# Kernel optimization log

Hardware: AMD Instinct MI355X
Metric: run time of the kernel (lower is better)

## Reference

```python
import jax, jax.numpy as jnp
import numpy as np

B, C_IN, C_OUT, N, T = 16, 32, 64, 1024, 24
IN_DIM, S_DIM, D_DIM, K, KT = 1, 16, 16, 3, 3


def conv1x1(x, W, b):
    # x: [B,Ci,N,T], W: [Co,Ci], b: [Co] -> [B,Co,N,T]
    return jnp.einsum('oi,bint->bont', W, x) + b[None, :, None, None]


def conv_t(x, W, b):
    # temporal conv, kernel (1,KT), padding (0,1) -> length preserved
    out = jax.lax.conv_general_dilated(
        x, W, window_strides=(1, 1), padding=((0, 0), (1, 1)),
        dimension_numbers=('NCHW', 'OIHW', 'NCHW'))
    return out + b[None, :, None, None]


def coss_attn(Dv, y, Wq, bq, Wk, bk, Wv, bv):
    # cross-attention per node over the temporal axis: Q from y, K/V from Dv
    Q = conv1x1(y, Wq, bq)
    Kx = conv1x1(Dv, Wk, bk)
    V = conv1x1(Dv, Wv, bv)
    scale = 1.0 / jnp.sqrt(jnp.asarray(Q.shape[1], Q.dtype))
    A = jax.nn.softmax(jnp.einsum('bcnt,bcns->bnts', Q, Kx) * scale, axis=-1)
    return jnp.einsum('bnts,bcns->bcnt', A, V)


def cheby(x, supports, Wg, bg, k):
    # Chebyshev polynomial graph conv: T0=I, T1=L, T2=2L T1 - T0
    n = supports.shape[0]
    L0 = jnp.eye(n, dtype=x.dtype)
    L1 = supports
    Ls = [L0, L1]
    for _ in range(2, k):
        L2 = 2.0 * supports @ L1 - L0
        L0, L1 = L1, L2
        Ls.append(L2)
    Lap = jnp.stack(Ls, 0)  # [K,N,N]
    xk = jnp.einsum('kqn,bcnt->bckqt', Lap, x)  # aggregate neighbours
    bsz, c, kk, nn, tt = xk.shape
    xk = xk.reshape(bsz, c * kk, nn, tt)
    return conv1x1(xk, Wg, bg)


def setup_inputs() -> dict:
    key = jax.random.key(0)
    ks = jax.random.split(key, 32)
    s = 0.05
    inp = {
        'x': jax.random.normal(ks[0], (B, C_IN, N, T), jnp.float32),
        'supports': jax.random.normal(ks[1], (N, N), jnp.float32) / np.sqrt(N).astype(np.float32),
        'CD': jax.random.normal(ks[2], (N, D_DIM), jnp.float32),
        'CS': jax.random.normal(ks[3], (N, S_DIM), jnp.float32),
        'adj': jax.random.normal(ks[4], (N, N), jnp.float32) / np.sqrt(N).astype(np.float32),
        # DelayEstimators params
        'W_de': jax.random.normal(ks[5], (C_OUT, C_IN), jnp.float32) * s,
        'b_de': jnp.zeros((C_OUT,), jnp.float32),
        'Wd': jax.random.normal(ks[6], (D_DIM, T), jnp.float32) * s,
        # conv_pro
        'W_pro': jax.random.normal(ks[7], (IN_DIM, C_IN), jnp.float32) * s,
        'b_pro': jnp.zeros((IN_DIM,), jnp.float32),
        # MultiScaleGCN
        'W_mii': jax.random.normal(ks[8], (C_OUT, S_DIM), jnp.float32) * s,
        'b_mii': jnp.zeros((C_OUT,), jnp.float32),
        # conv_1 residual
        'W_1': jax.random.normal(ks[9], (C_OUT, C_IN), jnp.float32) * s,
        'b_1': jnp.zeros((C_OUT,), jnp.float32),
        # TSFN cross-attention (query from x with c_in channels)
        'Wq_t': jax.random.normal(ks[10], (C_OUT, C_IN), jnp.float32) * s,
        'bq_t': jnp.zeros((C_OUT,), jnp.float32),
        'Wk_t': jax.random.normal(ks[11], (C_OUT, C_OUT), jnp.float32) * s,
        'bk_t': jnp.zeros((C_OUT,), jnp.float32),
        'Wv_t': jax.random.normal(ks[12], (C_OUT, C_OUT), jnp.float32) * s,
        'bv_t': jnp.zeros((C_OUT,), jnp.float32),
        # conv1 temporal (1,Kt)
        'W_c1': jax.random.normal(ks[13], (C_OUT, C_OUT, 1, KT), jnp.float32) * s,
        'b_c1': jnp.zeros((C_OUT,), jnp.float32),
        # SSFN cross-attention
        'Wq_s': jax.random.normal(ks[14], (C_OUT, C_OUT), jnp.float32) * s,
        'bq_s': jnp.zeros((C_OUT,), jnp.float32),
        'Wk_s': jax.random.normal(ks[15], (C_OUT, C_OUT), jnp.float32) * s,
        'bk_s': jnp.zeros((C_OUT,), jnp.float32),
        'Wv_s': jax.random.normal(ks[16], (C_OUT, C_OUT), jnp.float32) * s,
        'bv_s': jnp.zeros((C_OUT,), jnp.float32),
        # cheby conv output projection (K*c_out -> 2*c_out)
        'W_g': jax.random.normal(ks[17], (2 * C_OUT, K * C_OUT), jnp.float32) * s,
        'b_g': jnp.zeros((2 * C_OUT,), jnp.float32),
    }
    return inp


def reference(x, supports, CD, CS, adj, W_de, b_de, Wd, W_pro, b_pro,
              W_mii, b_mii, W_1, b_1, Wq_t, bq_t, Wk_t, bk_t, Wv_t, bv_t,
              W_c1, b_c1, Wq_s, bq_s, Wk_s, bk_s, Wv_s, bv_s, W_g, b_g):
    # DelayEstimators: projected trend modulated by node-wise learned delay gate
    delay = jax.nn.sigmoid(jnp.tanh(CD @ Wd))            # [N,T]
    D = conv1x1(x, W_de, b_de) * delay[None, None, :, :]  # [B,c_out,N,T]
    # conv_pro + broadcast of spatial context CS
    u = conv1x1(x, W_pro, b_pro)[:, 0]                    # [B,N,T] (in_dim==1)
    CSb = jnp.einsum('bnt,ne->bent', u, CS)               # [B,S_dim,N,T]
    # MultiScaleGCN: 1x1 projection + adjacency aggregation (identity + adj)
    h = conv1x1(CSb, W_mii, b_mii)
    S = h + jnp.einsum('nm,bcmt->bcnt', adj, h)           # [B,c_out,N,T]
    x_input1 = conv1x1(x, W_1, b_1)
    XD = coss_attn(D, x, Wq_t, bq_t, Wk_t, bk_t, Wv_t, bv_t) + x_input1
    x1 = conv_t(XD, W_c1, b_c1)
    XS = coss_attn(S, x1, Wq_s, bq_s, Wk_s, bk_s, Wv_s, bv_s)
    x2 = cheby(XS, supports, W_g, b_g, K)                 # [B,2*c_out,N,T]
    filt, gate = x2[:, :C_OUT], x2[:, C_OUT:]
    return (filt + x_input1) * jax.nn.sigmoid(gate)
```

## Files before the change

kernel.cpp:

```cpp
#include <hip/hip_runtime.h>
#include <cstdint>
#include <cstddef>

#define B_    16
#define CIN_  32
#define COUT_ 64
#define N_    1024
#define T_    24
#define SD_   16
#define DD_   16

#define NT_      (N_*T_)
#define BNT_     (B_*N_*T_)
#define UE_COLS  (B_*T_*SD_)
#define XS_COLS  (B_*COUT_*T_)
#define HALF_COLS (XS_COLS/2)

typedef unsigned short ushort_t;
using bf16x8 = __attribute__((ext_vector_type(8))) short;
using f32x4  = __attribute__((ext_vector_type(4))) float;

#define OFF_DELAY 0ul
#define OFF_M     98304ul
#define OFF_R     360448ul
#define OFF_U     364544ul
#define OFF_W1T   1953792ul
#define OFF_WGBF  2048000ul
#define OFF_SBF   2195456ul
#define OFF_ADJBF 4292608ul
#define OFF_STBF  6389760ul
#define OFF_L2BF  8486912ul
#define OFF_X1    10584064ul
#define OFF_X2    23166976ul
#define OFF_XS    48332800ul
#define OFF_Y1H   98664448ul
#define OFF_Y2H   123830272ul
#define OFF_WBF   148996096ul

#define WB_DE   0
#define WB_QT   2048
#define WB_1    4096
#define WB_MIIA 6144
#define WB_KT   8192
#define WB_VT   12288
#define WB_QS   16384
#define WB_KS   20480
#define WB_VS   24576
#define WB_C1A  28672
#define WB_TOTAL 40960

__device__ __forceinline__ float bfb2f(ushort_t h) {
  union { unsigned u; float f; } v; v.u = ((unsigned)h) << 16; return v.f;
}
__device__ __forceinline__ ushort_t f2bfb(float f) {
  union { float f; unsigned u; } v; v.f = f;
  unsigned u = v.u;
  return (ushort_t)((u + 0x7fffu + ((u >> 16) & 1u)) >> 16);
}
__device__ __forceinline__ float sigm_(float z) { return 1.f / (1.f + expf(-z)); }

__device__ __forceinline__ void gl_lds16(const ushort_t* g, ushort_t* l) {
  __builtin_amdgcn_global_load_lds(
      (const __attribute__((address_space(1))) unsigned int*)g,
      (__attribute__((address_space(3))) unsigned int*)l, 16, 0, 0);
}

__device__ __forceinline__ void st4bf(ushort_t* p, float v0, float v1, float v2, float v3) {
  uint2 w;
  w.x = (unsigned)f2bfb(v0) | ((unsigned)f2bfb(v1) << 16);
  w.y = (unsigned)f2bfb(v2) | ((unsigned)f2bfb(v3) << 16);
  *(uint2*)p = w;
}

__global__ __launch_bounds__(256) void k_prep(
    const float* __restrict__ supports, const float* __restrict__ adj,
    const float* __restrict__ W_de, const float* __restrict__ Wq_t,
    const float* __restrict__ W_1, const float* __restrict__ W_mii,
    const float* __restrict__ Wk_t, const float* __restrict__ Wv_t,
    const float* __restrict__ Wq_s, const float* __restrict__ Wk_s,
    const float* __restrict__ Wv_s, const float* __restrict__ W_c1,
    const float* __restrict__ W_g,
    ushort_t* __restrict__ Sbf, ushort_t* __restrict__ adjbf,
    float* __restrict__ W1T, ushort_t* __restrict__ WGBF,
    ushort_t* __restrict__ WBF)
{
  int idx = blockIdx.x * 256 + threadIdx.x;
  if (idx < N_*N_) {
    Sbf[idx]   = f2bfb(supports[idx]);
    adjbf[idx] = f2bfb(adj[idx]);
  }
  int j = idx - N_*N_;
  if (j < 0) return;
  if (j < 2048) { int k = j>>6, c = j&63; W1T[j] = W_1[c*32 + k]; return; }
  j -= 2048;
  if (j < 24576) { WGBF[j] = f2bfb(W_g[j]); return; }
  j -= 24576;
  if (j < 2048) { WBF[WB_DE + j] = f2bfb(W_de[j]); return; }
  j -= 2048;
  if (j < 2048) { WBF[WB_QT + j] = f2bfb(Wq_t[j]); return; }
  j -= 2048;
  if (j < 2048) { WBF[WB_1 + j] = f2bfb(W_1[j]); return; }
  j -= 2048;
  if (j < 2048) { int c = j>>5, k = j&31;
                  WBF[WB_MIIA + j] = (k < 16) ? f2bfb(W_mii[c*16 + k]) : (ushort_t)0; return; }
  j -= 2048;
  if (j < 4096) { WBF[WB_KT + j] = f2bfb(Wk_t[j]); return; }
  j -= 4096;
  if (j < 4096) { WBF[WB_VT + j] = f2bfb(Wv_t[j]); return; }
  j -= 4096;
  if (j < 4096) { WBF[WB_QS + j] = f2bfb(Wq_s[j]); return; }
  j -= 4096;
  if (j < 4096) { WBF[WB_KS + j] = f2bfb(Wk_s[j]); return; }
  j -= 4096;
  if (j < 4096) { WBF[WB_VS + j] = f2bfb(Wv_s[j]); return; }
  j -= 4096;
  if (j < 12288) { int d = j >> 12, r = j & 4095, c = r >> 6, jj = r & 63;
                   WBF[WB_C1A + j] = f2bfb(W_c1[(c*64 + jj)*3 + d]); return; }
}
#define PREP_TOTAL (N_*N_ + 2048 + 24576 + WB_TOTAL)

__global__ __launch_bounds__(256) void k_pre(
    const float* __restrict__ CD, const float* __restrict__ Wd,
    const float* __restrict__ CS, const float* __restrict__ W_mii,
    const float* __restrict__ adj,
    float* __restrict__ delay, float* __restrict__ Mbuf, float* __restrict__ Rbuf)
{
  int idx = blockIdx.x * 256 + threadIdx.x;
  if (idx < NT_) {
    int n = idx / T_, t = idx % T_;
    float z = 0.f;
    #pragma unroll
    for (int d = 0; d < DD_; ++d) z += CD[n*DD_ + d] * Wd[d*T_ + t];
    delay[idx] = sigm_(tanhf(z));
  }
  int i2 = idx - NT_;
  if (i2 >= 0 && i2 < N_*COUT_) {
    int n = i2 / COUT_, c = i2 % COUT_;
    float z = 0.f;
    #pragma unroll
    for (int e = 0; e < SD_; ++e) z += CS[n*SD_ + e] * W_mii[c*SD_ + e];
    Mbuf[i2] = z;
  }
  int i3 = idx - NT_ - N_*COUT_;
  if (i3 >= 0 && i3 < 8*N_) {
    int n = i3 >> 3, jl = i3 & 7;
    const float* row = adj + (size_t)n * N_;
    float s = 0.f;
    for (int m = jl; m < N_; m += 8) s += row[m];
    s += __shfl_xor(s, 1);
    s += __shfl_xor(s, 2);
    s += __shfl_xor(s, 4);
    if (jl == 0) Rbuf[n] = s;
  }
}

__global__ __launch_bounds__(256) void k_u(
    const float* __restrict__ x, const float* __restrict__ W_pro,
    const float* __restrict__ b_pro, const float* __restrict__ CS,
    float* __restrict__ u, ushort_t* __restrict__ Ue)
{
  int idx = blockIdx.x * 256 + threadIdx.x;
  if (idx >= BNT_) return;
  int t = idx % T_;
  int n = (idx / T_) % N_;
  int b = idx / (T_ * N_);
  const float* xp = x + ((size_t)b * CIN_ * N_ + n) * T_ + t;
  float z = b_pro[0];
  #pragma unroll
  for (int i = 0; i < CIN_; ++i) z += W_pro[i] * xp[(size_t)i * NT_];
  u[idx] = z;
  ushort_t* up = Ue + (size_t)n * UE_COLS + (b * T_ + t) * SD_;
  #pragma unroll
  for (int e = 0; e < SD_; ++e) up[e] = f2bfb(z * CS[n*SD_ + e]);
}

__global__ __launch_bounds__(256) void k_tr(
    const ushort_t* __restrict__ src, ushort_t* __restrict__ dst,
    int R, int sstride)
{
  __shared__ ushort_t tb[32][33];
  const int tid = threadIdx.x;
  const int tx = tid & 31, ty = tid >> 5;
  const int c0 = blockIdx.x * 32, r0 = blockIdx.y * 32;
  #pragma unroll
  for (int p = 0; p < 4; ++p) {
    int r = r0 + ty + p*8;
    tb[ty + p*8][tx] = src[(size_t)r * sstride + c0 + tx];
  }
  __syncthreads();
  #pragma unroll
  for (int p = 0; p < 4; ++p) {
    int c = c0 + ty + p*8;
    dst[(size_t)c * R + r0 + tx] = tb[tx][ty + p*8];
  }
}

template<int MODE>
__global__ __launch_bounds__(256) void k_mmx(
    const ushort_t* __restrict__ Abf, const ushort_t* __restrict__ BT,
    ushort_t* __restrict__ Cc, int ncols)
{
  __shared__ ushort_t As[128*64];
  __shared__ ushort_t Bs[128*64];
  const int tid  = threadIdx.x;
  const int wave = tid >> 6, lane = tid & 63;
  const int row0 = blockIdx.y * 128;
  const int col0 = blockIdx.x * 128;
  const int wm = (wave >> 1) * 64, wn = (wave & 1) * 64;
  const int l15 = lane & 15, quad = lane >> 4, l7 = lane & 7;

  f32x4 acc[4][4];
  #pragma unroll
  for (int i = 0; i < 4; ++i)
    #pragma unroll
    for (int j = 0; j < 4; ++j) acc[i][j] = (f32x4){0.f,0.f,0.f,0.f};

  for (int kb = 0; kb < 1024; kb += 64) {
    #pragma unroll
    for (int p = 0; p < 4; ++p) {
      int chunk = p*256 + tid;
      int r = chunk >> 3, pc = chunk & 7;
      int kc = pc ^ (r & 7);
      gl_lds16(Abf + (size_t)(row0 + r)*1024 + (kb + kc*8), &As[chunk*8]);
    }
    #pragma unroll
    for (int p = 0; p < 4; ++p) {
      int chunk = p*256 + tid;
      int r = chunk >> 3, pc = chunk & 7;
      int kc = pc ^ (r & 7);
      gl_lds16(BT + (size_t)(col0 + r)*1024 + (kb + kc*8), &Bs[chunk*8]);
    }
    __syncthreads();
    #pragma unroll
    for (int kh = 0; kh < 2; ++kh) {
      const int kcb = kh * 4;
      bf16x8 af[4], bfr[4];
      #pragma unroll
      for (int mi = 0; mi < 4; ++mi)
        af[mi] = *(const bf16x8*)&As[(wm + mi*16 + l15)*64 + (((kcb + quad) ^ l7) << 3)];
      #pragma unroll
      for (int ni = 0; ni < 4; ++ni)
        bfr[ni] = *(const bf16x8*)&Bs[(wn + ni*16 + l15)*64 + (((kcb + quad) ^ l7) << 3)];
      #pragma unroll
      for (int mi = 0; mi < 4; ++mi)
        #pragma unroll
        for (int ni = 0; ni < 4; ++ni)
          acc[mi][ni] = __builtin_amdgcn_mfma_f32_16x16x32_bf16(
              af[mi], bfr[ni], acc[mi][ni], 0, 0, 0);
    }
    __syncthreads();
  }

  #pragma unroll
  for (int mi = 0; mi < 4; ++mi) {
    int grow_b = row0 + wm + mi*16 + quad*4;
    #pragma unroll
    for (int ni = 0; ni < 4; ++ni) {
      int gcol = col0 + wn + ni*16 + l15;
      #pragma unroll
      for (int j = 0; j < 4; ++j) {
        float v = acc[mi][ni][j];
        int grow = grow_b + j;
        if (MODE == 2) v = 2.f*v - ((grow == gcol) ? 1.f : 0.f);
        Cc[(size_t)grow * ncols + gcol] = f2bfb(v);
      }
    }
  }
}

__global__ __launch_bounds__(256) void k_mmy(
    const ushort_t* __restrict__ Sbf, const ushort_t* __restrict__ L2bf,
    const ushort_t* __restrict__ BT,
    ushort_t* __restrict__ Y1, ushort_t* __restrict__ Y2, int ncols)
{
  __shared__ ushort_t As[128*64];
  __shared__ ushort_t Bs[128*64];
  const int tid  = threadIdx.x;
  const int wave = tid >> 6, lane = tid & 63;
  const bool isY2 = blockIdx.y >= 8;
  const ushort_t* Abf = isY2 ? L2bf : Sbf;
  ushort_t* Cc = isY2 ? Y2 : Y1;
  const int row0 = (blockIdx.y & 7) * 128;
  const int col0 = blockIdx.x * 128;
  const int wm = (wave >> 1) * 64, wn = (wave & 1) * 64;
  const int l15 = lane & 15, quad = lane >> 4, l7 = lane & 7;

  f32x4 acc[4][4];
  #pragma unroll
  for (int i = 0; i < 4; ++i)
    #pragma unroll
    for (int j = 0; j < 4; ++j) acc[i][j] = (f32x4){0.f,0.f,0.f,0.f};

  for (int kb = 0; kb < 1024; kb += 64) {
    #pragma unroll
    for (int p = 0; p < 4; ++p) {
      int chunk = p*256 + tid;
      int r = chunk >> 3, pc = chunk & 7;
      int kc = pc ^ (r & 7);
      gl_lds16(Abf + (size_t)(row0 + r)*1024 + (kb + kc*8), &As[chunk*8]);
    }
    #pragma unroll
    for (int p = 0; p < 4; ++p) {
      int chunk = p*256 + tid;
      int r = chunk >> 3, pc = chunk & 7;
      int kc = pc ^ (r & 7);
      gl_lds16(BT + (size_t)(col0 + r)*1024 + (kb + kc*8), &Bs[chunk*8]);
    }
    __syncthreads();
    #pragma unroll
    for (int kh = 0; kh < 2; ++kh) {
      const int kcb = kh * 4;
      bf16x8 af[4], bfr[4];
      #pragma unroll
      for (int mi = 0; mi < 4; ++mi)
        af[mi] = *(const bf16x8*)&As[(wm + mi*16 + l15)*64 + (((kcb + quad) ^ l7) << 3)];
      #pragma unroll
      for (int ni = 0; ni < 4; ++ni)
        bfr[ni] = *(const bf16x8*)&Bs[(wn + ni*16 + l15)*64 + (((kcb + quad) ^ l7) << 3)];
      #pragma unroll
      for (int mi = 0; mi < 4; ++mi)
        #pragma unroll
        for (int ni = 0; ni < 4; ++ni)
          acc[mi][ni] = __builtin_amdgcn_mfma_f32_16x16x32_bf16(
              af[mi], bfr[ni], acc[mi][ni], 0, 0, 0);
    }
    __syncthreads();
  }

  #pragma unroll
  for (int mi = 0; mi < 4; ++mi) {
    int grow_b = row0 + wm + mi*16 + quad*4;
    #pragma unroll
    for (int ni = 0; ni < 4; ++ni) {
      int gcol = col0 + wn + ni*16 + l15;
      #pragma unroll
      for (int j = 0; j < 4; ++j)
        Cc[(size_t)(grow_b + j) * ncols + gcol] = f2bfb(acc[mi][ni][j]);
    }
  }
}

#define SW 72
__global__ __launch_bounds__(256, 6) void k_attn_mfma(
    const float* __restrict__ x,
    const float* __restrict__ delay, const float* __restrict__ Mbuf,
    const float* __restrict__ Rbuf, const float* __restrict__ u,
    const ushort_t* __restrict__ P,
    const ushort_t* __restrict__ WBF,
    const float* __restrict__ b_de, const float* __restrict__ bq_t,
    const float* __restrict__ b_1,  const float* __restrict__ b_mii,
    const float* __restrict__ bk_t, const float* __restrict__ bv_t,
    const float* __restrict__ bq_s, const float* __restrict__ bk_s,
    const float* __restrict__ bv_s, const float* __restrict__ b_c1,
    ushort_t* __restrict__ XS)
{
  const int n = blockIdx.x, b = blockIdx.y;
  const int tid = threadIdx.x, wave = tid >> 6, lane = tid & 63;
  const int l15 = lane & 15, quad = lane >> 4;

  __shared__ __align__(16) char smem[24352];
  ushort_t* bufQ = (ushort_t*)(smem + 0);
  ushort_t* XDg  = (ushort_t*)(smem + 0);
  ushort_t* Bc   = (ushort_t*)(smem + 4896);
  ushort_t* bufK = (ushort_t*)(smem + 4896);
  ushort_t* bufD = (ushort_t*)(smem + 9504);
  ushort_t* scb  = (ushort_t*)(smem + 9504);
  ushort_t* Sts  = (ushort_t*)(smem + 14112);
  ushort_t* V2   = (ushort_t*)(smem + 18720);
  ushort_t* Pts  = (ushort_t*)(smem + 18720);
  float* delay_s = (float*)(smem + 23840);
  float* urow    = (float*)(smem + 23968);
  float* Mrow    = (float*)(smem + 24096);

  for (int i = tid; i < 768; i += 256) {
    int ci = i / 24, t = i - ci*24;
    Bc[t*SW + ci] = f2bfb(x[(((size_t)b*CIN_ + ci)*N_ + n)*T_ + t]);
  }
  for (int i = tid; i < 768; i += 256) {
    int t = i >> 5, e = i & 31;
    Pts[t*40 + e] = (e < 16) ? P[(size_t)n*UE_COLS + (b*T_ + t)*SD_ + e] : (ushort_t)0;
  }
  if (tid < 32)       urow[tid] = (tid < 24) ? u[((size_t)b*N_ + n)*T_ + tid] : 0.f;
  else if (tid < 64)  { int t = tid - 32; delay_s[t] = (t < 24) ? delay[n*T_ + t] : 0.f; }
  else if (tid < 128) Mrow[tid - 64] = Mbuf[n*COUT_ + (tid - 64)];
  __syncthreads();

  const int c0 = wave * 16;
  const float Rn = Rbuf[n];
  float x1r[2][4];

  {
    bf16x8 aD = *(const bf16x8*)(WBF + WB_DE   + (c0+l15)*32 + quad*8);
    bf16x8 aQ = *(const bf16x8*)(WBF + WB_QT   + (c0+l15)*32 + quad*8);
    bf16x8 a1w = *(const bf16x8*)(WBF + WB_1   + (c0+l15)*32 + quad*8);
    bf16x8 aS = *(const bf16x8*)(WBF + WB_MIIA + (c0+l15)*32 + quad*8);
    float4 bD4 = *(const float4*)&b_de [c0 + quad*4];
    float4 bQ4 = *(const float4*)&bq_t [c0 + quad*4];
    float4 b14 = *(const float4*)&b_1  [c0 + quad*4];
    float4 bS4 = *(const float4*)&b_mii[c0 + quad*4];
    float4 Mv4 = *(const float4*)&Mrow [c0 + quad*4];
    float bD[4] = {bD4.x,bD4.y,bD4.z,bD4.w};
    float bQ[4] = {bQ4.x,bQ4.y,bQ4.z,bQ4.w};
    float b1a[4] = {b14.x,b14.y,b14.z,b14.w};
    float bS[4] = {bS4.x,bS4.y,bS4.z,bS4.w};
    float Mv[4] = {Mv4.x,Mv4.y,Mv4.z,Mv4.w};
    #pragma unroll
    for (int nt = 0; nt < 2; ++nt) {
      int bt = nt*16 + l15;
      bf16x8 bx = *(const bf16x8*)&Bc[bt*SW + quad*8];
      bf16x8 bp = *(const bf16x8*)&Pts[bt*40 + quad*8];
      f32x4 z = {0.f,0.f,0.f,0.f};
      f32x4 accD = __builtin_amdgcn_mfma_f32_16x16x32_bf16(aD, bx, z, 0,0,0);
      f32x4 accQ = __builtin_amdgcn_mfma_f32_16x16x32_bf16(aQ, bx, z, 0,0,0);
      f32x4 acc1 = __builtin_amdgcn_mfma_f32_16x16x32_bf16(a1w, bx, z, 0,0,0);
      f32x4 accS = __builtin_amdgcn_mfma_f32_16x16x32_bf16(aS, bp, z, 0,0,0);
      float dl = delay_s[bt], ut = urow[bt];
      st4bf(&bufD[bt*SW + c0 + quad*4],
            (accD[0]+bD[0])*dl, (accD[1]+bD[1])*dl, (accD[2]+bD[2])*dl, (accD[3]+bD[3])*dl);
      st4bf(&bufQ[bt*SW + c0 + quad*4],
            accQ[0]+bQ[0], accQ[1]+bQ[1], accQ[2]+bQ[2], accQ[3]+bQ[3]);
      #pragma unroll
      for (int r = 0; r < 4; ++r) x1r[nt][r] = acc1[r] + b1a[r];
      st4bf(&Sts[bt*SW + c0 + quad*4],
            accS[0] + ut*Mv[0] + bS[0]*(1.f+Rn), accS[1] + ut*Mv[1] + bS[1]*(1.f+Rn),
            accS[2] + ut*Mv[2] + bS[2]*(1.f+Rn), accS[3] + ut*Mv[3] + bS[3]*(1.f+Rn));
    }
  }
  __syncthreads();

  {
    for (int i = tid; i < 512; i += 256) V2[(i>>3)*40 + 24 + (i&7)] = 0;
    bf16x8 aK0 = *(const bf16x8*)(WBF + WB_KT + (c0+l15)*64 + quad*8);
    bf16x8 aK1 = *(const bf16x8*)(WBF + WB_KT + (c0+l15)*64 + 32 + quad*8);
    bf16x8 aV0 = *(const bf16x8*)(WBF + WB_VT + (c0+l15)*64 + quad*8);
    bf16x8 aV1 = *(const bf16x8*)(WBF + WB_VT + (c0+l15)*64 + 32 + quad*8);
    float4 bK4 = *(const float4*)&bk_t[c0 + quad*4];
    float4 bV4 = *(const float4*)&bv_t[c0 + quad*4];
    float bK[4] = {bK4.x,bK4.y,bK4.z,bK4.w};
    float bV[4] = {bV4.x,bV4.y,bV4.z,bV4.w};
    #pragma unroll
    for (int nt = 0; nt < 2; ++nt) {
      int bt = nt*16 + l15;
      bf16x8 b0 = *(const bf16x8*)&bufD[bt*SW + quad*8];
      bf16x8 b1v = *(const bf16x8*)&bufD[bt*SW + 32 + quad*8];
      f32x4 accK = {0.f,0.f,0.f,0.f}, accV = {0.f,0.f,0.f,0.f};
      accK = __builtin_amdgcn_mfma_f32_16x16x32_bf16(aK0, b0,  accK, 0,0,0);
      accK = __builtin_amdgcn_mfma_f32_16x16x32_bf16(aK1, b1v, accK, 0,0,0);
      accV = __builtin_amdgcn_mfma_f32_16x16x32_bf16(aV0, b0,  accV, 0,0,0);
      accV = __builtin_amdgcn_mfma_f32_16x16x32_bf16(aV1, b1v, accV, 0,0,0);
      st4bf(&bufK[bt*SW + c0 + quad*4],
            accK[0]+bK[0], accK[1]+bK[1], accK[2]+bK[2], accK[3]+bK[3]);
      if (bt < 24) {
        #pragma unroll
        for (int r = 0; r < 4; ++r)
          V2[(c0 + quad*4 + r)*40 + bt] = f2bfb(accV[r] + bV[r]);
      }
    }
  }
  __syncthreads();

  if (wave < 2) {
    const int mt = wave * 16;
    bf16x8 a0 = *(const bf16x8*)&bufQ[(mt+l15)*SW + quad*8];
    bf16x8 a1f = *(const bf16x8*)&bufQ[(mt+l15)*SW + 32 + quad*8];
    bf16x8 k0a = *(const bf16x8*)&bufK[l15*SW + quad*8];
    bf16x8 k0b = *(const bf16x8*)&bufK[l15*SW + 32 + quad*8];
    bf16x8 k1a = *(const bf16x8*)&bufK[(16+l15)*SW + quad*8];
    bf16x8 k1b = *(const bf16x8*)&bufK[(16+l15)*SW + 32 + quad*8];
    f32x4 s0 = {0.f,0.f,0.f,0.f}, s1 = {0.f,0.f,0.f,0.f};
    s0 = __builtin_amdgcn_mfma_f32_16x16x32_bf16(a0, k0a, s0, 0,0,0);
    s0 = __builtin_amdgcn_mfma_f32_16x16x32_bf16(a1f, k0b, s0, 0,0,0);
    s1 = __builtin_amdgcn_mfma_f32_16x16x32_bf16(a0, k1a, s1, 0,0,0);
    s1 = __builtin_amdgcn_mfma_f32_16x16x32_bf16(a1f, k1b, s1, 0,0,0);
    #pragma unroll
    for (int r = 0; r < 4; ++r) {
      float v0 = 0.125f * s0[r];
      float v1 = (l15 < 8) ? 0.125f * s1[r] : -3.0e38f;
      float mx = fmaxf(v0, v1);
      mx = fmaxf(mx, __shfl_xor(mx, 1));
      mx = fmaxf(mx, __shfl_xor(mx, 2));
      mx = fmaxf(mx, __shfl_xor(mx, 4));
      mx = fmaxf(mx, __shfl_xor(mx, 8));
      float e0 = expf(v0 - mx);
      float e1 = (l15 < 8) ? expf(v1 - mx) : 0.f;
      float sm = e0 + e1;
      sm += __shfl_xor(sm, 1);
      sm += __shfl_xor(sm, 2);
      sm += __shfl_xor(sm, 4);
      sm += __shfl_xor(sm, 8);
      float inv = 1.f / sm;
      int t = mt + quad*4 + r;
      bool tv = (t < 24);
      scb[t*40 + l15]      = tv ? f2bfb(e0 * inv) : (ushort_t)0;
      scb[t*40 + 16 + l15] = (tv && l15 < 8) ? f2bfb(e1 * inv) : (ushort_t)0;
    }
  }
  __syncthreads();

  {
    for (int i = tid; i < 640; i += 256) {
      int r = i >> 6, cg = i & 63;
      int row = (r == 0) ? 0 : (24 + r);
      XDg[row*SW + cg] = 0;
    }
    bf16x8 aV = *(const bf16x8*)&V2[(c0 + l15)*40 + quad*8];
    #pragma unroll
    for (int nt = 0; nt < 2; ++nt) {
      bf16x8 bP = *(const bf16x8*)&scb[(nt*16 + l15)*40 + quad*8];
      f32x4 z = {0.f,0.f,0.f,0.f};
      f32x4 acc = __builtin_amdgcn_mfma_f32_16x16x32_bf16(aV, bP, z, 0,0,0);
      int t = nt*16 + l15;
      if (t < 24) {
        #pragma unroll
        for (int r = 0; r < 4; ++r)
          XDg[(1 + t)*SW + c0 + quad*4 + r] = f2bfb(acc[r] + x1r[nt][r]);
      }
    }
  }
  __syncthreads();

  {
    float4 bc4 = *(const float4*)&b_c1[c0 + quad*4];
    float bc[4] = {bc4.x,bc4.y,bc4.z,bc4.w};
    f32x4 acc0 = {0.f,0.f,0.f,0.f}, acc1v = {0.f,0.f,0.f,0.f};
    #pragma unroll
    for (int d = 0; d < 3; ++d) {
      const ushort_t* Ad = WBF + WB_C1A + d*4096;
      bf16x8 a0 = *(const bf16x8*)(Ad + (c0+l15)*64 + quad*8);
      bf16x8 a1f = *(const bf16x8*)(Ad + (c0+l15)*64 + 32 + quad*8);
      {
        int rr = 0*16 + l15 + d;
        bf16x8 b0 = *(const bf16x8*)&XDg[rr*SW + quad*8];
        bf16x8 b1f = *(const bf16x8*)&XDg[rr*SW + 32 + quad*8];
        acc0 = __builtin_amdgcn_mfma_f32_16x16x32_bf16(a0, b0, acc0, 0,0,0);
        acc0 = __builtin_amdgcn_mfma_f32_16x16x32_bf16(a1f, b1f, acc0, 0,0,0);
      }
      {
        int rr = 1*16 + l15 + d;
        bf16x8 b0 = *(const bf16x8*)&XDg[rr*SW + quad*8];
        bf16x8 b1f = *(const bf16x8*)&XDg[rr*SW + 32 + quad*8];
        acc1v = __builtin_amdgcn_mfma_f32_16x16x32_bf16(a0, b0, acc1v, 0,0,0);
        acc1v = __builtin_amdgcn_mfma_f32_16x16x32_bf16(a1f, b1f, acc1v, 0,0,0);
      }
    }
    st4bf(&bufD[(0*16 + l15)*SW + c0 + quad*4],
          acc0[0]+bc[0], acc0[1]+bc[1], acc0[2]+bc[2], acc0[3]+bc[3]);
    st4bf(&bufD[(1*16 + l15)*SW + c0 + quad*4],
          acc1v[0]+bc[0], acc1v[1]+bc[1], acc1v[2]+bc[2], acc1v[3]+bc[3]);
  }
  __syncthreads();

  {
    bf16x8 aq0 = *(const bf16x8*)(WBF + WB_QS + (c0+l15)*64 + quad*8);
    bf16x8 aq1 = *(const bf16x8*)(WBF + WB_QS + (c0+l15)*64 + 32 + quad*8);
    bf16x8 ak0 = *(const bf16x8*)(WBF + WB_KS + (c0+l15)*64 + quad*8);
    bf16x8 ak1 = *(const bf16x8*)(WBF + WB_KS + (c0+l15)*64 + 32 + quad*8);
    bf16x8 av0 = *(const bf16x8*)(WBF + WB_VS + (c0+l15)*64 + quad*8);
    bf16x8 av1 = *(const bf16x8*)(WBF + WB_VS + (c0+l15)*64 + 32 + quad*8);
    float4 bq4 = *(const float4*)&bq_s[c0 + quad*4];
    float4 bk4 = *(const float4*)&bk_s[c0 + quad*4];
    float4 bv4 = *(const float4*)&bv_s[c0 + quad*4];
    float bq[4] = {bq4.x,bq4.y,bq4.z,bq4.w};
    float bk[4] = {bk4.x,bk4.y,bk4.z,bk4.w};
    float bv[4] = {bv4.x,bv4.y,bv4.z,bv4.w};
    #pragma unroll
    for (int nt = 0; nt < 2; ++nt) {
      int bt = nt*16 + l15;
      bf16x8 bx0 = *(const bf16x8*)&bufD[bt*SW + quad*8];
      bf16x8 bx1 = *(const bf16x8*)&bufD[bt*SW + 32 + quad*8];
      bf16x8 bs0 = *(const bf16x8*)&Sts[bt*SW + quad*8];
      bf16x8 bs1 = *(const bf16x8*)&Sts[bt*SW + 32 + quad*8];
      f32x4 accQ = {0.f,0.f,0.f,0.f}, accK = {0.f,0.f,0.f,0.f}, accV = {0.f,0.f,0.f,0.f};
      accQ = __builtin_amdgcn_mfma_f32_16x16x32_bf16(aq0, bx0, accQ, 0,0,0);
      accQ = __builtin_amdgcn_mfma_f32_16x16x32_bf16(aq1, bx1, accQ, 0,0,0);
      accK = __builtin_amdgcn_mfma_f32_16x16x32_bf16(ak0, bs0, accK, 0,0,0);
      accK = __builtin_amdgcn_mfma_f32_16x16x32_bf16(ak1, bs1, accK, 0,0,0);
      accV = __builtin_amdgcn_mfma_f32_16x16x32_bf16(av0, bs0, accV, 0,0,0);
      accV = __builtin_amdgcn_mfma_f32_16x16x32_bf16(av1, bs1, accV, 0,0,0);
      st4bf(&bufQ[bt*SW + c0 + quad*4],
            accQ[0]+bq[0], accQ[1]+bq[1], accQ[2]+bq[2], accQ[3]+bq[3]);
      st4bf(&bufK[bt*SW + c0 + quad*4],
            accK[0]+bk[0], accK[1]+bk[1], accK[2]+bk[2], accK[3]+bk[3]);
      if (bt < 24) {
        #pragma unroll
        for (int r = 0; r < 4; ++r)
          V2[(c0 + quad*4 + r)*40 + bt] = f2bfb(accV[r] + bv[r]);
      }
    }
  }
  __syncthreads();

  if (wave < 2) {
    const int mt = wave * 16;
    bf16x8 a0 = *(const bf16x8*)&bufQ[(mt+l15)*SW + quad*8];
    bf16x8 a1f = *(const bf16x8*)&bufQ[(mt+l15)*SW + 32 + quad*8];
    bf16x8 k0a = *(const bf16x8*)&bufK[l15*SW + quad*8];
    bf16x8 k0b = *(const bf16x8*)&bufK[l15*SW + 32 + quad*8];
    bf16x8 k1a = *(const bf16x8*)&bufK[(16+l15)*SW + quad*8];
    bf16x8 k1b = *(const bf16x8*)&bufK[(16+l15)*SW + 32 + quad*8];
    f32x4 s0 = {0.f,0.f,0.f,0.f}, s1 = {0.f,0.f,0.f,0.f};
    s0 = __builtin_amdgcn_mfma_f32_16x16x32_bf16(a0, k0a, s0, 0,0,0);
    s0 = __builtin_amdgcn_mfma_f32_16x16x32_bf16(a1f, k0b, s0, 0,0,0);
    s1 = __builtin_amdgcn_mfma_f32_16x16x32_bf16(a0, k1a, s1, 0,0,0);
    s1 = __builtin_amdgcn_mfma_f32_16x16x32_bf16(a1f, k1b, s1, 0,0,0);
    #pragma unroll
    for (int r = 0; r < 4; ++r) {
      float v0 = 0.125f * s0[r];
      float v1 = (l15 < 8) ? 0.125f * s1[r] : -3.0e38f;
      float mx = fmaxf(v0, v1);
      mx = fmaxf(mx, __shfl_xor(mx, 1));
      mx = fmaxf(mx, __shfl_xor(mx, 2));
      mx = fmaxf(mx, __shfl_xor(mx, 4));
      mx = fmaxf(mx, __shfl_xor(mx, 8));
      float e0 = expf(v0 - mx);
      float e1 = (l15 < 8) ? expf(v1 - mx) : 0.f;
      float sm = e0 + e1;
      sm += __shfl_xor(sm, 1);
      sm += __shfl_xor(sm, 2);
      sm += __shfl_xor(sm, 4);
      sm += __shfl_xor(sm, 8);
      float inv = 1.f / sm;
      int t = mt + quad*4 + r;
      bool tv = (t < 24);
      scb[t*40 + l15]      = tv ? f2bfb(e0 * inv) : (ushort_t)0;
      scb[t*40 + 16 + l15] = (tv && l15 < 8) ? f2bfb(e1 * inv) : (ushort_t)0;
    }
  }
  __syncthreads();

  {
    int nc = wave * 16;
    bf16x8 bv0 = *(const bf16x8*)&V2[(nc + l15)*40 + quad*8];
    #pragma unroll
    for (int mt = 0; mt < 2; ++mt) {
      bf16x8 af = *(const bf16x8*)&scb[(mt*16 + l15)*40 + quad*8];
      f32x4 z = {0.f,0.f,0.f,0.f};
      f32x4 acc = __builtin_amdgcn_mfma_f32_16x16x32_bf16(af, bv0, z, 0,0,0);
      int ccol = nc + l15;
      int t0 = mt*16 + quad*4;
      if (t0 < 24) {
        uint2 w;
        w.x = (unsigned)f2bfb(acc[0]) | ((unsigned)f2bfb(acc[1]) << 16);
        w.y = (unsigned)f2bfb(acc[2]) | ((unsigned)f2bfb(acc[3]) << 16);
        *(uint2*)(XS + (size_t)n*XS_COLS + (size_t)b*COUT_*T_ + ccol*T_ + t0) = w;
      }
    }
  }
}

#define ZW 200
__global__ __launch_bounds__(256) void k_final(
    const float* __restrict__ x,
    const ushort_t* __restrict__ XS, const ushort_t* __restrict__ Y1h,
    const ushort_t* __restrict__ Y2h,
    const ushort_t* __restrict__ WGBF,
    const float* __restrict__ W1T, const float* __restrict__ b_1,
    const float* __restrict__ b_g,
    int h, float* __restrict__ out)
{
  const int n = blockIdx.x, bb = blockIdx.y, tid = threadIdx.x;
  const int b = h * 8 + bb;
  const int wave = tid >> 6, lane = tid & 63;
  const int l15 = lane & 15, quad = lane >> 4;

  __shared__ __align__(16) ushort_t Zt[32*ZW];
  __shared__ float x1sh[COUT_*T_];
  __shared__ float xts[CIN_*T_];

  size_t baseg = (size_t)n * XS_COLS + (size_t)b * COUT_ * T_;
  size_t baseh = (size_t)n * HALF_COLS + (size_t)bb * COUT_ * T_;

  for (int i = tid; i < 8*ZW; i += 256) Zt[24*ZW + i] = 0;
  for (int i = tid; i < COUT_*T_; i += 256) {
    int c = i / T_, t = i - c*T_;
    ushort_t* zr = &Zt[t*ZW + 3*c];
    zr[0] = XS [baseg + i];
    zr[1] = Y1h[baseh + i];
    zr[2] = Y2h[baseh + i];
  }
  for (int i = tid; i < CIN_*T_; i += 256) {
    int ci = i / T_, t = i - ci*T_;
    xts[i] = x[(((size_t)b * CIN_ + ci) * N_ + n) * T_ + t];
  }
  __syncthreads();

  {
    const int c = tid >> 2, tq = tid & 3;
    float a[6];
    #pragma unroll
    for (int m = 0; m < 6; ++m) a[m] = b_1[c];
    for (int i = 0; i < CIN_; ++i) {
      float w = W1T[i*64 + c];
      #pragma unroll
      for (int m = 0; m < 6; ++m) a[m] += w * xts[i*T_ + tq + 4*m];
    }
    #pragma unroll
    for (int m = 0; m < 6; ++m) x1sh[c*T_ + tq + 4*m] = a[m];
  }

  f32x4 accF[2] = {{0.f,0.f,0.f,0.f},{0.f,0.f,0.f,0.f}};
  f32x4 accG[2] = {{0.f,0.f,0.f,0.f},{0.f,0.f,0.f,0.f}};
  const ushort_t* WF = WGBF + (size_t)(wave*16 + l15)*192 + quad*8;
  const ushort_t* WG = WF + 64*192;
  #pragma unroll
  for (int ks = 0; ks < 6; ++ks) {
    bf16x8 wf = *(const bf16x8*)(WF + ks*32);
    bf16x8 wg = *(const bf16x8*)(WG + ks*32);
    #pragma unroll
    for (int nt = 0; nt < 2; ++nt) {
      bf16x8 bz = *(const bf16x8*)&Zt[(nt*16 + l15)*ZW + ks*32 + quad*8];
      accF[nt] = __builtin_amdgcn_mfma_f32_16x16x32_bf16(wf, bz, accF[nt], 0,0,0);
      accG[nt] = __builtin_amdgcn_mfma_f32_16x16x32_bf16(wg, bz, accG[nt], 0,0,0);
    }
  }
  __syncthreads();

  {
    float4 bgF4 = *(const float4*)&b_g[wave*16 + quad*4];
    float4 bgG4 = *(const float4*)&b_g[64 + wave*16 + quad*4];
    float bgF[4] = {bgF4.x, bgF4.y, bgF4.z, bgF4.w};
    float bgG[4] = {bgG4.x, bgG4.y, bgG4.z, bgG4.w};
    #pragma unroll
    for (int nt = 0; nt < 2; ++nt) {
      int t = nt*16 + l15;
      if (t < 24) {
        #pragma unroll
        for (int r = 0; r < 4; ++r) {
          int c = wave*16 + quad*4 + r;
          float fv = accF[nt][r] + bgF[r] + x1sh[c*T_ + t];
          float gv = accG[nt][r] + bgG[r];
          out[(((size_t)b * COUT_ + c) * N_ + n) * T_ + t] = fv * sigm_(gv);
        }
      }
    }
  }
}

extern "C" void kernel_launch(void* const* d_in, const int* in_sizes, int n_in,
                              void* d_out, int out_size, void* d_ws, size_t ws_size,
                              hipStream_t stream) {
  const float* x        = (const float*)d_in[0];
  const float* supports = (const float*)d_in[1];
  const float* CD       = (const float*)d_in[2];
  const float* CS       = (const float*)d_in[3];
  const float* adj      = (const float*)d_in[4];
  const float* W_de  = (const float*)d_in[5];  const float* b_de  = (const float*)d_in[6];
  const float* Wd    = (const float*)d_in[7];
  const float* W_pro = (const float*)d_in[8];  const float* b_pro = (const float*)d_in[9];
  const float* W_mii = (const float*)d_in[10]; const float* b_mii = (const float*)d_in[11];
  const float* W_1   = (const float*)d_in[12]; const float* b_1   = (const float*)d_in[13];
  const float* Wq_t  = (const float*)d_in[14]; const float* bq_t  = (const float*)d_in[15];
  const float* Wk_t  = (const float*)d_in[16]; const float* bk_t  = (const float*)d_in[17];
  const float* Wv_t  = (const float*)d_in[18]; const float* bv_t  = (const float*)d_in[19];
  const float* W_c1  = (const float*)d_in[20]; const float* b_c1  = (const float*)d_in[21];
  const float* Wq_s  = (const float*)d_in[22]; const float* bq_s  = (const float*)d_in[23];
  const float* Wk_s  = (const float*)d_in[24]; const float* bk_s  = (const float*)d_in[25];
  const float* Wv_s  = (const float*)d_in[26]; const float* bv_s  = (const float*)d_in[27];
  const float* W_g   = (const float*)d_in[28]; const float* b_g   = (const float*)d_in[29];
  float* out = (float*)d_out;

  char* ws = (char*)d_ws;
  float*    delay = (float*)(ws + OFF_DELAY);
  float*    Mbuf  = (float*)(ws + OFF_M);
  float*    Rbuf  = (float*)(ws + OFF_R);
  float*    u     = (float*)(ws + OFF_U);
  float*    W1T   = (float*)(ws + OFF_W1T);
  ushort_t* WGBF  = (ushort_t*)(ws + OFF_WGBF);
  ushort_t* Sbf   = (ushort_t*)(ws + OFF_SBF);
  ushort_t* adjbf = (ushort_t*)(ws + OFF_ADJBF);
  ushort_t* STbf  = (ushort_t*)(ws + OFF_STBF);
  ushort_t* L2bf  = (ushort_t*)(ws + OFF_L2BF);
  ushort_t* Ue    = (ushort_t*)(ws + OFF_X1);
  ushort_t* P     = (ushort_t*)(ws + OFF_X1);
  ushort_t* UeT   = (ushort_t*)(ws + OFF_X2);
  ushort_t* XST   = (ushort_t*)(ws + OFF_X2);
  ushort_t* XS    = (ushort_t*)(ws + OFF_XS);
  ushort_t* Y1h   = (ushort_t*)(ws + OFF_Y1H);
  ushort_t* Y2h   = (ushort_t*)(ws + OFF_Y2H);
  ushort_t* WBF   = (ushort_t*)(ws + OFF_WBF);

  (void)in_sizes; (void)n_in; (void)out_size; (void)ws_size;

  k_prep<<<dim3((PREP_TOTAL + 255)/256), 256, 0, stream>>>(
      supports, adj, W_de, Wq_t, W_1, W_mii, Wk_t, Wv_t, Wq_s, Wk_s, Wv_s,
      W_c1, W_g, Sbf, adjbf, W1T, WGBF, WBF);
  k_pre<<<dim3((NT_ + N_*COUT_ + 8*N_ + 255)/256), 256, 0, stream>>>(
      CD, Wd, CS, W_mii, adj, delay, Mbuf, Rbuf);
  k_tr<<<dim3(N_/32, N_/32), 256, 0, stream>>>(Sbf, STbf, N_, N_);
  k_mmx<2><<<dim3(8, 8), 256, 0, stream>>>(Sbf, STbf, L2bf, 1024);
  k_u<<<dim3((BNT_ + 255)/256), 256, 0, stream>>>(x, W_pro, b_pro, CS, u, Ue);
  k_tr<<<dim3(UE_COLS/32, N_/32), 256, 0, stream>>>(Ue, UeT, N_, UE_COLS);
  k_mmx<0><<<dim3(UE_COLS/128, N_/128), 256, 0, stream>>>(adjbf, UeT, P, UE_COLS);
  k_attn_mfma<<<dim3(N_, B_), 256, 0, stream>>>(
      x, delay, Mbuf, Rbuf, u, P, WBF,
      b_de, bq_t, b_1, b_mii, bk_t, bv_t, bq_s, bk_s, bv_s, b_c1, XS);
  for (int h = 0; h < 2; ++h) {
    k_tr<<<dim3(HALF_COLS/32, N_/32), 256, 0, stream>>>(
        XS + (size_t)h * HALF_COLS, XST, N_, XS_COLS);
    k_mmy<<<dim3(HALF_COLS/128, 16), 256, 0, stream>>>(
        Sbf, L2bf, XST, Y1h, Y2h, HALF_COLS);
    k_final<<<dim3(N_, 8), 256, 0, stream>>>(
        x, XS, Y1h, Y2h, WGBF, W1T, b_1, b_g, h, out);
  }
}
```

Baseline: 775.4 us.

## Vectorize bf16 packing, load P directly into MFMA operands, use fast exp

Adds a paired bf16 round-and-pack helper that replaces the per-element conversions in st4bf, the XS store and k_u. k_u now writes its 16 Ue values with two 16-byte stores instead of 16 scalar stores. The fused attention kernel drops the LDS staging of P (Pts) and its loop, loading the MFMA B operand straight from global memory and zero-filling the upper quads. expf is replaced with __expf in the softmax and sigmoid, trading a little accuracy for cheaper transcendentals.

```diff
diff --git a/kernel.cpp b/kernel.cpp
--- a/kernel.cpp
+++ b/kernel.cpp
@@ -57,7 +57,14 @@
   unsigned u = v.u;
   return (ushort_t)((u + 0x7fffu + ((u >> 16) & 1u)) >> 16);
 }
-__device__ __forceinline__ float sigm_(float z) { return 1.f / (1.f + expf(-z)); }
+__device__ __forceinline__ unsigned rne2(float lo, float hi) {
+  union { float f; unsigned u; } a, b;
+  a.f = lo; b.f = hi;
+  unsigned ua = (a.u + 0x7fffu + ((a.u >> 16) & 1u)) >> 16;
+  unsigned ub = (b.u + 0x7fffu + ((b.u >> 16) & 1u)) & 0xffff0000u;
+  return ua | ub;
+}
+__device__ __forceinline__ float sigm_(float z) { return 1.f / (1.f + __expf(-z)); }
 
 __device__ __forceinline__ void gl_lds16(const ushort_t* g, ushort_t* l) {
   __builtin_amdgcn_global_load_lds(
@@ -67,8 +74,8 @@
 
 __device__ __forceinline__ void st4bf(ushort_t* p, float v0, float v1, float v2, float v3) {
   uint2 w;
-  w.x = (unsigned)f2bfb(v0) | ((unsigned)f2bfb(v1) << 16);
-  w.y = (unsigned)f2bfb(v2) | ((unsigned)f2bfb(v3) << 16);
+  w.x = rne2(v0, v1);
+  w.y = rne2(v2, v3);
   *(uint2*)p = w;
 }
 
@@ -170,8 +177,12 @@
   for (int i = 0; i < CIN_; ++i) z += W_pro[i] * xp[(size_t)i * NT_];
   u[idx] = z;
   ushort_t* up = Ue + (size_t)n * UE_COLS + (b * T_ + t) * SD_;
+  unsigned w[8];
   #pragma unroll
-  for (int e = 0; e < SD_; ++e) up[e] = f2bfb(z * CS[n*SD_ + e]);
+  for (int e = 0; e < 8; ++e)
+    w[e] = rne2(z * CS[n*SD_ + 2*e], z * CS[n*SD_ + 2*e + 1]);
+  ((uint4*)up)[0] = make_uint4(w[0], w[1], w[2], w[3]);
+  ((uint4*)up)[1] = make_uint4(w[4], w[5], w[6], w[7]);
 }
 
 __global__ __launch_bounds__(256) void k_tr(
@@ -367,7 +378,6 @@
   ushort_t* scb  = (ushort_t*)(smem + 9504);
   ushort_t* Sts  = (ushort_t*)(smem + 14112);
   ushort_t* V2   = (ushort_t*)(smem + 18720);
-  ushort_t* Pts  = (ushort_t*)(smem + 18720);
   float* delay_s = (float*)(smem + 23840);
   float* urow    = (float*)(smem + 23968);
   float* Mrow    = (float*)(smem + 24096);
@@ -375,10 +385,6 @@
   for (int i = tid; i < 768; i += 256) {
     int ci = i / 24, t = i - ci*24;
     Bc[t*SW + ci] = f2bfb(x[(((size_t)b*CIN_ + ci)*N_ + n)*T_ + t]);
-  }
-  for (int i = tid; i < 768; i += 256) {
-    int t = i >> 5, e = i & 31;
-    Pts[t*40 + e] = (e < 16) ? P[(size_t)n*UE_COLS + (b*T_ + t)*SD_ + e] : (ushort_t)0;
   }
   if (tid < 32)       urow[tid] = (tid < 24) ? u[((size_t)b*N_ + n)*T_ + tid] : 0.f;
   else if (tid < 64)  { int t = tid - 32; delay_s[t] = (t < 24) ? delay[n*T_ + t] : 0.f; }
@@ -408,7 +414,9 @@
     for (int nt = 0; nt < 2; ++nt) {
       int bt = nt*16 + l15;
       bf16x8 bx = *(const bf16x8*)&Bc[bt*SW + quad*8];
-      bf16x8 bp = *(const bf16x8*)&Pts[bt*40 + quad*8];
+      bf16x8 bp = (bf16x8){0,0,0,0,0,0,0,0};
+      if (quad < 2)
+        bp = *(const bf16x8*)(P + (size_t)n*UE_COLS + (b*T_ + bt)*SD_ + quad*8);
       f32x4 z = {0.f,0.f,0.f,0.f};
       f32x4 accD = __builtin_amdgcn_mfma_f32_16x16x32_bf16(aD, bx, z, 0,0,0);
       f32x4 accQ = __builtin_amdgcn_mfma_f32_16x16x32_bf16(aQ, bx, z, 0,0,0);
@@ -481,8 +489,8 @@
       mx = fmaxf(mx, __shfl_xor(mx, 2));
       mx = fmaxf(mx, __shfl_xor(mx, 4));
       mx = fmaxf(mx, __shfl_xor(mx, 8));
-      float e0 = expf(v0 - mx);
-      float e1 = (l15 < 8) ? expf(v1 - mx) : 0.f;
+      float e0 = __expf(v0 - mx);
+      float e1 = (l15 < 8) ? __expf(v1 - mx) : 0.f;
       float sm = e0 + e1;
       sm += __shfl_xor(sm, 1);
       sm += __shfl_xor(sm, 2);
@@ -612,8 +620,8 @@
       mx = fmaxf(mx, __shfl_xor(mx, 2));
       mx = fmaxf(mx, __shfl_xor(mx, 4));
       mx = fmaxf(mx, __shfl_xor(mx, 8));
-      float e0 = expf(v0 - mx);
-      float e1 = (l15 < 8) ? expf(v1 - mx) : 0.f;
+      float e0 = __expf(v0 - mx);
+      float e1 = (l15 < 8) ? __expf(v1 - mx) : 0.f;
       float sm = e0 + e1;
       sm += __shfl_xor(sm, 1);
       sm += __shfl_xor(sm, 2);
@@ -640,8 +648,8 @@
       int t0 = mt*16 + quad*4;
       if (t0 < 24) {
         uint2 w;
-        w.x = (unsigned)f2bfb(acc[0]) | ((unsigned)f2bfb(acc[1]) << 16);
-        w.y = (unsigned)f2bfb(acc[2]) | ((unsigned)f2bfb(acc[3]) << 16);
+        w.x = rne2(acc[0], acc[1]);
+        w.y = rne2(acc[2], acc[3]);
         *(uint2*)(XS + (size_t)n*XS_COLS + (size_t)b*COUT_*T_ + ccol*T_ + t0) = w;
       }
     }
```

New measurement: 776.9 us. About the same (+0.2%).
